# Optimization experiments

Hardware: AMD Instinct MI355X
Metric: run time of the kernel (lower is better)

## Reference

```python
import jax, jax.numpy as jnp
import numpy as np
import math

V, S, D, B = 50257, 2048, 512, 4
DFF = 4 * D
EPS = 1e-5


def layer_norm(z, g, b):
    mu = jnp.mean(z, axis=-1, keepdims=True)
    var = jnp.mean((z - mu) ** 2, axis=-1, keepdims=True)
    return (z - mu) * jax.lax.rsqrt(var + EPS) * g + b


def pos_embedding(seq_len, d_model):
    # Faithful to get_positional_value: angle = pos / 10000**(2*i/d), sin for even i, cos for odd i
    pos = jnp.arange(seq_len, dtype=jnp.float32)[:, None]          # [S,1]
    i = jnp.arange(d_model, dtype=jnp.float32)[None, :]            # [1,D]
    ang = pos / jnp.power(10000.0, 2.0 * i / d_model)              # [S,D]
    even = (jnp.arange(d_model) % 2 == 0)[None, :]
    return jnp.where(even, jnp.sin(ang), jnp.cos(ang))


def setup_inputs() -> dict:
    key = jax.random.key(0)
    ks = jax.random.split(key, 14)
    w = lambda k, sh: jax.random.normal(k, sh, dtype=jnp.float32) * 0.02
    return {
        "input_seq": jax.random.randint(ks[0], (B, S), 0, V),
        "emb": w(ks[1], (V, D)),
        "wk": w(ks[2], (D, D)), "bk": jnp.zeros((D,), jnp.float32),
        "wq": w(ks[3], (D, D)), "bq": jnp.zeros((D,), jnp.float32),
        "wv": w(ks[4], (D, D)), "bv": jnp.zeros((D,), jnp.float32),
        "ln_g": jnp.ones((D,), jnp.float32), "ln_b": jnp.zeros((D,), jnp.float32),
        "w1": w(ks[5], (D, DFF)), "b1": jnp.zeros((DFF,), jnp.float32),
        "w2": w(ks[6], (DFF, D)), "b2": jnp.zeros((D,), jnp.float32),
    }


def reference(input_seq, emb, wk, bk, wq, bq, wv, bv, ln_g, ln_b, w1, b1, w2, b2):
    x = emb[input_seq]                                              # [B,S,D]
    x = (x + pos_embedding(S, D)) * math.sqrt(D)
    # NB original passes (k, q, v) into Attention(Q, K, V), so Q:=k_proj, K:=q_proj, V:=v_proj
    k = x @ wk + bk
    q = x @ wq + bq
    v = x @ wv + bv
    scores = jnp.einsum("bid,bjd->bij", k, q) / math.sqrt(D)        # [B,S,S]
    attn = jax.nn.softmax(scores, axis=-1) @ v                      # [B,S,D]
    r = layer_norm(x + attn, ln_g, ln_b)
    ff = jax.nn.gelu(r @ w1 + b1, approximate=False) @ w2 + b2
    out = layer_norm(r + ff, ln_g, ln_b)                            # shared LN params (same module reused)
    return out
```

## Files before the change

kernel.cpp:

```cpp
#include <hip/hip_runtime.h>
#include <math.h>

static constexpr int BB  = 4;
static constexpr int S   = 2048;
static constexpr int D   = 512;
static constexpr int DFF = 2048;
static constexpr int BS  = BB * S;

using v8h = __attribute__((ext_vector_type(8))) _Float16;
using v4h = __attribute__((ext_vector_type(4))) _Float16;
using v2h = __attribute__((ext_vector_type(2))) _Float16;
using v4f = __attribute__((ext_vector_type(4))) float;

__device__ __forceinline__ void async16(const void* g, void* l) {
  __builtin_amdgcn_global_load_lds(
      (const __attribute__((address_space(1))) unsigned int*)g,
      (__attribute__((address_space(3))) unsigned int*)l, 16, 0, 0);
}

__device__ __forceinline__ float blockSum(float v) {
#pragma unroll
  for (int o = 32; o; o >>= 1) v += __shfl_xor(v, o, 64);
  __shared__ float t[4];
  __syncthreads();
  if ((threadIdx.x & 63) == 0) t[threadIdx.x >> 6] = v;
  __syncthreads();
  return t[0] + t[1] + t[2] + t[3];
}
__device__ __forceinline__ float blockMax(float v) {
#pragma unroll
  for (int o = 32; o; o >>= 1) v = fmaxf(v, __shfl_xor(v, o, 64));
  __shared__ float t[4];
  __syncthreads();
  if ((threadIdx.x & 63) == 0) t[threadIdx.x >> 6] = v;
  __syncthreads();
  return fmaxf(fmaxf(t[0], t[1]), fmaxf(t[2], t[3]));
}

__global__ __launch_bounds__(256) void embed_pos_k(
    const int* __restrict__ seq, const float* __restrict__ emb,
    float* __restrict__ X, _Float16* __restrict__ Xh) {
  const int bs = blockIdx.x;
  const int s  = bs & (S - 1);
  const int idx = seq[bs];
  const float* er = emb + (size_t)idx * D;
  const float cexp = -0.05190512648261504f;
  const int d0 = threadIdx.x * 2;
  const float2 e2 = *(const float2*)&er[d0];
  const float a0 = (float)s * exp2f((float)d0 * cexp);
  const float a1 = (float)s * exp2f((float)(d0 + 1) * cexp);
  const float v0 = (e2.x + sinf(a0)) * 22.62741699796952f;
  const float v1 = (e2.y + cosf(a1)) * 22.62741699796952f;
  const size_t o = (size_t)bs * D + d0;
  *(float2*)&X[o] = make_float2(v0, v1);
  *(v2h*)&Xh[o] = v2h{(_Float16)v0, (_Float16)v1};
}

__global__ __launch_bounds__(256) void prep_k(
    const float* __restrict__ wk, const float* __restrict__ wq,
    const float* __restrict__ wv, const float* __restrict__ w1,
    const float* __restrict__ w2, const float* __restrict__ bk,
    const float* __restrict__ bq, const float* __restrict__ bv,
    _Float16* __restrict__ wcat, _Float16* __restrict__ w1T,
    _Float16* __restrict__ w2T, float* __restrict__ bcat) {
  const int idx = blockIdx.x * 256 + threadIdx.x;
  if (idx < 786432) {
    const int which = idx >> 18, e = idx & 262143;
    const int k = e >> 9, n = e & 511;
    const float* w = (which == 0) ? wk : (which == 1) ? wq : wv;
    wcat[((long)(which * 512 + n)) * 512 + k] = (_Float16)w[e];
  } else if (idx < 786432 + 1048576) {
    const int e = idx - 786432;
    const int k = e >> 11, n = e & 2047;
    w1T[(long)n * 512 + k] = (_Float16)w1[e];
  } else if (idx < 786432 + 2097152) {
    const int e = idx - 786432 - 1048576;
    const int k = e >> 9, n = e & 511;
    w2T[(long)n * 2048 + k] = (_Float16)w2[e];
  } else if (idx < 786432 + 2097152 + 1536) {
    const int e = idx - 786432 - 2097152;
    const float* b = (e < 512) ? bk : (e < 1024) ? bq : bv;
    bcat[e] = b[e & 511];
  }
}

template <int TM, int OMODE, int ACT>
__global__ __launch_bounds__(256) void mm_k(
    const _Float16* __restrict__ Ap, const _Float16* __restrict__ Bp,
    void* __restrict__ Cp, void* __restrict__ Cp2, void* __restrict__ Cp3,
    const float* __restrict__ bias,
    int N, int K, long sA, long sB, long sC, float scale) {
  constexpr int ATE = TM * 64;
  constexpr int BTE = 128 * 64;
  constexpr int TILE = ATE + BTE;
  __shared__ __align__(16) _Float16 lds[2 * TILE];

  const int tid = threadIdx.x, lane = tid & 63, w = tid >> 6;
  const int quad = lane >> 4, l16 = lane & 15;
  constexpr int MT = 4;
  constexpr int NT = (TM == 128) ? 4 : 2;
  constexpr int WN = (TM == 128) ? 64 : 32;
  const int wm = (TM == 128) ? (w >> 1) : 0;
  const int wn = (TM == 128) ? (w & 1) : w;
  const int m0 = blockIdx.y * TM, n0 = blockIdx.x * 128;

  const _Float16* A = Ap + (long)blockIdx.z * sA;
  const _Float16* B = Bp + (long)blockIdx.z * sB;

  v4f acc[MT][NT] = {};
  const int srow8 = lane >> 3;
  const int cs = (lane & 7) ^ srow8;
  const int lsw = l16 & 7;

  auto stage = [&](int k0, int half) {
    _Float16* Ah = lds + half * TILE;
    _Float16* Bh = Ah + ATE;
#pragma unroll
    for (int i = 0; i < TM / 32; ++i) {
      const int is = w + i * 4;
      async16(A + (long)(m0 + is * 8 + srow8) * K + k0 + cs * 8, Ah + is * 512);
    }
#pragma unroll
    for (int i = 0; i < 4; ++i) {
      const int is = w + i * 4;
      async16(B + (long)(n0 + is * 8 + srow8) * K + k0 + cs * 8, Bh + is * 512);
    }
  };

  stage(0, 0);
  __syncthreads();

  const int nK = K >> 6;
  for (int t = 0; t < nK; ++t) {
    const int cur = t & 1;
    if (t + 1 < nK) stage((t + 1) << 6, cur ^ 1);

    const _Float16* Ah = lds + cur * TILE;
    const _Float16* Bh = Ah + ATE;

    v8h af[MT][2], bfr[NT][2];
#pragma unroll
    for (int mt = 0; mt < MT; ++mt) {
      const int rr = wm * 64 + mt * 16 + l16;
#pragma unroll
      for (int kk = 0; kk < 2; ++kk) {
        const int c = (kk * 4 + quad) ^ lsw;
        af[mt][kk] = *(v8h*)&Ah[rr * 64 + c * 8];
      }
    }
#pragma unroll
    for (int nt = 0; nt < NT; ++nt) {
      const int rn = wn * WN + nt * 16 + l16;
#pragma unroll
      for (int kk = 0; kk < 2; ++kk) {
        const int c = (kk * 4 + quad) ^ lsw;
        bfr[nt][kk] = *(v8h*)&Bh[rn * 64 + c * 8];
      }
    }
#pragma unroll
    for (int kk = 0; kk < 2; ++kk)
#pragma unroll
      for (int mt = 0; mt < MT; ++mt)
#pragma unroll
        for (int nt = 0; nt < NT; ++nt)
          acc[mt][nt] = __builtin_amdgcn_mfma_f32_16x16x32_f16(
              af[mt][kk], bfr[nt][kk], acc[mt][nt], 0, 0, 0);

    __syncthreads();
  }

  const long Cz = (long)blockIdx.z * sC;
  const int region = n0 >> 9;
#pragma unroll
  for (int nt = 0; nt < NT; ++nt) {
    const int gn = n0 + wn * WN + nt * 16 + l16;
    const int gnl = gn & 511;
    const float bv = bias ? bias[gn] : 0.0f;
#pragma unroll
    for (int mt = 0; mt < MT; ++mt) {
      const int gmb = m0 + wm * 64 + mt * 16 + quad * 4;
      if constexpr (OMODE == 4) {
        if (region == 2) {
          const int z2 = gmb >> 11, ml = gmb & 2047;
          v4h h4;
#pragma unroll
          for (int r = 0; r < 4; ++r)
            h4[r] = (_Float16)(acc[mt][nt][r] * scale + bv);
          *(v4h*)&((_Float16*)Cp3)[((long)z2 * 512 + gnl) * 2048 + ml] = h4;
          continue;
        }
      }
#pragma unroll
      for (int r = 0; r < 4; ++r) {
        const int gm = gmb + r;
        float v = acc[mt][nt][r] * scale + bv;
        if constexpr (ACT == 1)
          v = 0.5f * v * (1.0f + erff(v * 0.7071067811865476f));
        if constexpr (OMODE == 0) {
          ((float*)Cp)[Cz + (long)gm * N + gn] = v;
        } else if constexpr (OMODE == 1) {
          ((_Float16*)Cp)[Cz + (long)gm * N + gn] = (_Float16)v;
        } else {
          if (region == 0) {
            ((_Float16*)Cp)[(long)gm * 512 + gnl] = (_Float16)v;
          } else {
            ((_Float16*)Cp2)[(long)gm * 512 + gnl] = (_Float16)v;
          }
        }
      }
    }
  }
}

__global__ __launch_bounds__(256) void mm64p_k(
    const _Float16* __restrict__ Ap, const _Float16* __restrict__ Bp,
    float* __restrict__ Cp, const float* __restrict__ bias,
    int N, int K, long sA, long sB, long sC, float scale) {
  constexpr int ATE = 64 * 64;
  constexpr int BTE = 128 * 64;
  constexpr int TILE = ATE + BTE;
  __shared__ __align__(16) _Float16 lds[3 * TILE];

  const int tid = threadIdx.x, lane = tid & 63, w = tid >> 6;
  const int quad = lane >> 4, l16 = lane & 15;
  const int m0 = blockIdx.y * 64, n0 = blockIdx.x * 128;

  const _Float16* A = Ap + (long)blockIdx.z * sA;
  const _Float16* B = Bp + (long)blockIdx.z * sB;

  v4f acc[4][2] = {};
  const int srow8 = lane >> 3;
  const int cs = (lane & 7) ^ srow8;
  const int lsw = l16 & 7;

  auto stage = [&](int t) {
    _Float16* Ah = lds + (t % 3) * TILE;
    _Float16* Bh = Ah + ATE;
    const int k0 = t << 6;
#pragma unroll
    for (int i = 0; i < 2; ++i) {
      const int is = w + i * 4;
      async16(A + (long)(m0 + is * 8 + srow8) * K + k0 + cs * 8, Ah + is * 512);
    }
#pragma unroll
    for (int i = 0; i < 4; ++i) {
      const int is = w + i * 4;
      async16(B + (long)(n0 + is * 8 + srow8) * K + k0 + cs * 8, Bh + is * 512);
    }
  };

  const int nK = K >> 6;
  stage(0);
  stage(1);

  for (int t = 0; t < nK; ++t) {
    __builtin_amdgcn_s_barrier();
    if (t + 2 < nK) {
      stage(t + 2);
      asm volatile("s_waitcnt vmcnt(12)" ::: "memory");
    } else if (t + 1 < nK) {
      asm volatile("s_waitcnt vmcnt(6)" ::: "memory");
    } else {
      asm volatile("s_waitcnt vmcnt(0)" ::: "memory");
    }
    __builtin_amdgcn_s_barrier();

    const _Float16* Ah = lds + (t % 3) * TILE;
    const _Float16* Bh = Ah + ATE;

    v8h af[4][2], bfr[2][2];
#pragma unroll
    for (int mt = 0; mt < 4; ++mt) {
      const int rr = mt * 16 + l16;
#pragma unroll
      for (int kk = 0; kk < 2; ++kk) {
        const int c = (kk * 4 + quad) ^ lsw;
        af[mt][kk] = *(v8h*)&Ah[rr * 64 + c * 8];
      }
    }
#pragma unroll
    for (int nt = 0; nt < 2; ++nt) {
      const int rn = w * 32 + nt * 16 + l16;
#pragma unroll
      for (int kk = 0; kk < 2; ++kk) {
        const int c = (kk * 4 + quad) ^ lsw;
        bfr[nt][kk] = *(v8h*)&Bh[rn * 64 + c * 8];
      }
    }
#pragma unroll
    for (int kk = 0; kk < 2; ++kk)
#pragma unroll
      for (int mt = 0; mt < 4; ++mt)
#pragma unroll
        for (int nt = 0; nt < 2; ++nt)
          acc[mt][nt] = __builtin_amdgcn_mfma_f32_16x16x32_f16(
              af[mt][kk], bfr[nt][kk], acc[mt][nt], 0, 0, 0);
  }

  const long Cz = (long)blockIdx.z * sC;
#pragma unroll
  for (int nt = 0; nt < 2; ++nt) {
    const int gn = n0 + w * 32 + nt * 16 + l16;
    const float bv = bias ? bias[gn] : 0.0f;
#pragma unroll
    for (int mt = 0; mt < 4; ++mt) {
      const int gmb = m0 + mt * 16 + quad * 4;
#pragma unroll
      for (int r = 0; r < 4; ++r) {
        const int gm = gmb + r;
        Cp[Cz + (long)gm * N + gn] = acc[mt][nt][r] * scale + bv;
      }
    }
  }
}

__global__ __launch_bounds__(256) void softmax_k(_Float16* __restrict__ Sc) {
  _Float16* p = Sc + (size_t)blockIdx.x * S;
  const int base = threadIdx.x * 8;
  const v8h a = *(const v8h*)(p + base);
  float v[8];
#pragma unroll
  for (int i = 0; i < 8; ++i) v[i] = (float)a[i];
  float m = -1e30f;
#pragma unroll
  for (int i = 0; i < 8; ++i) m = fmaxf(m, v[i]);
  m = blockMax(m);
  float sum = 0.f;
#pragma unroll
  for (int i = 0; i < 8; ++i) {
    v[i] = exp2f((v[i] - m) * 1.44269504f);
    sum += v[i];
  }
  sum = blockSum(sum);
  const float inv = 1.0f / sum;
  v8h o;
#pragma unroll
  for (int i = 0; i < 8; ++i) o[i] = (_Float16)(v[i] * inv);
  *(v8h*)(p + base) = o;
}

__global__ __launch_bounds__(256) void ln_res_k(
    float* __restrict__ X, const float* __restrict__ Add,
    const float* __restrict__ g, const float* __restrict__ b,
    _Float16* __restrict__ rF) {
  float* xr = X + (size_t)blockIdx.x * D;
  const float* ar = Add + (size_t)blockIdx.x * D;
  _Float16* rf = rF + (size_t)blockIdx.x * D;
  const int d0 = threadIdx.x * 2;
  const float2 xv = *(const float2*)&xr[d0];
  const float2 av = *(const float2*)&ar[d0];
  const float z0 = xv.x + av.x;
  const float z1 = xv.y + av.y;
  const float mu = blockSum(z0 + z1) * (1.0f / D);
  const float dd0 = z0 - mu, dd1 = z1 - mu;
  const float var = blockSum(dd0 * dd0 + dd1 * dd1) * (1.0f / D);
  const float rs = rsqrtf(var + 1e-5f);
  const float2 gv = *(const float2*)&g[d0];
  const float2 bv = *(const float2*)&b[d0];
  const float v0 = dd0 * rs * gv.x + bv.x;
  const float v1 = dd1 * rs * gv.y + bv.y;
  *(float2*)&xr[d0] = make_float2(v0, v1);
  *(v2h*)&rf[d0] = v2h{(_Float16)v0, (_Float16)v1};
}

__global__ __launch_bounds__(256) void ln_out_k(
    const float* __restrict__ R, const float* __restrict__ F,
    const float* __restrict__ g, const float* __restrict__ b,
    float* __restrict__ out) {
  const float* rr = R + (size_t)blockIdx.x * D;
  const float* fr = F + (size_t)blockIdx.x * D;
  float* orow = out + (size_t)blockIdx.x * D;
  const int d0 = threadIdx.x * 2;
  const float2 rv = *(const float2*)&rr[d0];
  const float2 fv = *(const float2*)&fr[d0];
  const float z0 = rv.x + fv.x;
  const float z1 = rv.y + fv.y;
  const float mu = blockSum(z0 + z1) * (1.0f / D);
  const float dd0 = z0 - mu, dd1 = z1 - mu;
  const float var = blockSum(dd0 * dd0 + dd1 * dd1) * (1.0f / D);
  const float rs = rsqrtf(var + 1e-5f);
  const float2 gv = *(const float2*)&g[d0];
  const float2 bv = *(const float2*)&b[d0];
  *(float2*)&orow[d0] =
      make_float2(dd0 * rs * gv.x + bv.x, dd1 * rs * gv.y + bv.y);
}

extern "C" void kernel_launch(void* const* d_in, const int* in_sizes, int n_in,
                              void* d_out, int out_size, void* d_ws, size_t ws_size,
                              hipStream_t stream) {
  (void)in_sizes; (void)n_in; (void)out_size; (void)ws_size;
  const int*   seq = (const int*)d_in[0];
  const float* emb = (const float*)d_in[1];
  const float* wk  = (const float*)d_in[2];
  const float* bk  = (const float*)d_in[3];
  const float* wq  = (const float*)d_in[4];
  const float* bq  = (const float*)d_in[5];
  const float* wv  = (const float*)d_in[6];
  const float* bv  = (const float*)d_in[7];
  const float* lng = (const float*)d_in[8];
  const float* lnb = (const float*)d_in[9];
  const float* w1  = (const float*)d_in[10];
  const float* b1  = (const float*)d_in[11];
  const float* w2  = (const float*)d_in[12];
  const float* b2  = (const float*)d_in[13];

  const size_t MBy = 1024 * 1024;
  char* wsb = (char*)d_ws;
  float*    X    = (float*)wsb;
  _Float16* Xh   = (_Float16*)(wsb + 16 * MBy);
  _Float16* kF   = (_Float16*)(wsb + 24 * MBy);
  _Float16* qF   = (_Float16*)(wsb + 32 * MBy);
  _Float16* vT   = (_Float16*)(wsb + 40 * MBy);
  _Float16* Sc   = (_Float16*)(wsb + 48 * MBy);
  float*    attn = (float*)(wsb + 81 * MBy);
  _Float16* rF   = (_Float16*)(wsb + 24 * MBy);
  _Float16* hF   = (_Float16*)(wsb + 48 * MBy);
  float*    ff   = (float*)(wsb + 32 * MBy);
  _Float16* wcat = (_Float16*)(wsb + 100 * MBy);
  float*    bcat = (float*)(wsb + 102 * MBy);
  _Float16* w1T  = (_Float16*)(wsb + 103 * MBy);
  _Float16* w2T  = (_Float16*)(wsb + 105 * MBy);

  const long SD = (long)S * D, SSl = (long)S * S;

  prep_k<<<11270, 256, 0, stream>>>(wk, wq, wv, w1, w2, bk, bq, bv,
                                    wcat, w1T, w2T, bcat);
  embed_pos_k<<<BS, 256, 0, stream>>>(seq, emb, X, Xh);

  mm_k<128, 4, 0><<<dim3(12, 64, 1), 256, 0, stream>>>(
      Xh, wcat, kF, qF, vT, bcat, 1536, D, 0, 0, 0, 1.0f);

  mm_k<128, 1, 0><<<dim3(16, 16, BB), 256, 0, stream>>>(
      kF, qF, Sc, nullptr, nullptr, nullptr, S, D, SD, SD, SSl,
      0.044194173824159216f);

  softmax_k<<<BS, 256, 0, stream>>>(Sc);

  mm64p_k<<<dim3(4, 32, BB), 256, 0, stream>>>(
      Sc, vT, attn, nullptr, D, S, SSl, (long)D * S, SD, 1.0f);

  ln_res_k<<<BS, 256, 0, stream>>>(X, attn, lng, lnb, rF);

  mm_k<128, 1, 1><<<dim3(16, 64, 1), 256, 0, stream>>>(
      rF, w1T, hF, nullptr, nullptr, b1, DFF, D, 0, 0, 0, 1.0f);
  mm64p_k<<<dim3(4, 128, 1), 256, 0, stream>>>(
      hF, w2T, ff, b2, D, DFF, 0, 0, 0, 1.0f);

  ln_out_k<<<BS, 256, 0, stream>>>(X, ff, lng, lnb, (float*)d_out);
}
```

Measured before the change: 365.6 us.

## Replace 128-tile GEMM with 256x256 tile, 512-thread kernel and vmcnt-based pipelining

After: 427.6 us. 16.9% more time.

```diff
diff --git a/kernel.cpp b/kernel.cpp
--- a/kernel.cpp
+++ b/kernel.cpp
@@ -84,73 +84,62 @@
   }
 }
 
-template <int TM, int OMODE, int ACT>
-__global__ __launch_bounds__(256) void mm_k(
+template <int OMODE, int ACT>
+__global__ __launch_bounds__(512, 2) void mm256p_k(
     const _Float16* __restrict__ Ap, const _Float16* __restrict__ Bp,
     void* __restrict__ Cp, void* __restrict__ Cp2, void* __restrict__ Cp3,
     const float* __restrict__ bias,
     int N, int K, long sA, long sB, long sC, float scale) {
-  constexpr int ATE = TM * 64;
-  constexpr int BTE = 128 * 64;
-  constexpr int TILE = ATE + BTE;
+  constexpr int ATE = 256 * 64;
+  constexpr int TILE = 2 * ATE;
   __shared__ __align__(16) _Float16 lds[2 * TILE];
 
   const int tid = threadIdx.x, lane = tid & 63, w = tid >> 6;
   const int quad = lane >> 4, l16 = lane & 15;
-  constexpr int MT = 4;
-  constexpr int NT = (TM == 128) ? 4 : 2;
-  constexpr int WN = (TM == 128) ? 64 : 32;
-  const int wm = (TM == 128) ? (w >> 1) : 0;
-  const int wn = (TM == 128) ? (w & 1) : w;
-  const int m0 = blockIdx.y * TM, n0 = blockIdx.x * 128;
+  const int wm = w >> 2, wn = w & 3;
+  const int m0 = blockIdx.y * 256, n0 = blockIdx.x * 256;
 
   const _Float16* A = Ap + (long)blockIdx.z * sA;
   const _Float16* B = Bp + (long)blockIdx.z * sB;
 
-  v4f acc[MT][NT] = {};
+  v4f acc[8][4] = {};
   const int srow8 = lane >> 3;
   const int cs = (lane & 7) ^ srow8;
   const int lsw = l16 & 7;
 
-  auto stage = [&](int k0, int half) {
+  auto stage = [&](int t, int half) {
     _Float16* Ah = lds + half * TILE;
     _Float16* Bh = Ah + ATE;
-#pragma unroll
-    for (int i = 0; i < TM / 32; ++i) {
-      const int is = w + i * 4;
+    const int k0 = t << 6;
+#pragma unroll
+    for (int i = 0; i < 4; ++i) {
+      const int is = w + i * 8;
       async16(A + (long)(m0 + is * 8 + srow8) * K + k0 + cs * 8, Ah + is * 512);
-    }
-#pragma unroll
-    for (int i = 0; i < 4; ++i) {
-      const int is = w + i * 4;
       async16(B + (long)(n0 + is * 8 + srow8) * K + k0 + cs * 8, Bh + is * 512);
     }
   };
 
   stage(0, 0);
-  __syncthreads();
 
   const int nK = K >> 6;
   for (int t = 0; t < nK; ++t) {
     const int cur = t & 1;
-    if (t + 1 < nK) stage((t + 1) << 6, cur ^ 1);
+    __builtin_amdgcn_s_barrier();
+    if (t + 1 < nK) {
+      stage(t + 1, cur ^ 1);
+      asm volatile("s_waitcnt vmcnt(8)" ::: "memory");
+    } else {
+      asm volatile("s_waitcnt vmcnt(0)" ::: "memory");
+    }
+    __builtin_amdgcn_s_barrier();
 
     const _Float16* Ah = lds + cur * TILE;
     const _Float16* Bh = Ah + ATE;
 
-    v8h af[MT][2], bfr[NT][2];
-#pragma unroll
-    for (int mt = 0; mt < MT; ++mt) {
-      const int rr = wm * 64 + mt * 16 + l16;
-#pragma unroll
-      for (int kk = 0; kk < 2; ++kk) {
-        const int c = (kk * 4 + quad) ^ lsw;
-        af[mt][kk] = *(v8h*)&Ah[rr * 64 + c * 8];
-      }
-    }
-#pragma unroll
-    for (int nt = 0; nt < NT; ++nt) {
-      const int rn = wn * WN + nt * 16 + l16;
+    v8h bfr[4][2];
+#pragma unroll
+    for (int nt = 0; nt < 4; ++nt) {
+      const int rn = wn * 64 + nt * 16 + l16;
 #pragma unroll
       for (int kk = 0; kk < 2; ++kk) {
         const int c = (kk * 4 + quad) ^ lsw;
@@ -158,27 +147,33 @@
       }
     }
 #pragma unroll
-    for (int kk = 0; kk < 2; ++kk)
-#pragma unroll
-      for (int mt = 0; mt < MT; ++mt)
-#pragma unroll
-        for (int nt = 0; nt < NT; ++nt)
+    for (int mt = 0; mt < 8; ++mt) {
+      const int rr = wm * 128 + mt * 16 + l16;
+      v8h af[2];
+#pragma unroll
+      for (int kk = 0; kk < 2; ++kk) {
+        const int c = (kk * 4 + quad) ^ lsw;
+        af[kk] = *(v8h*)&Ah[rr * 64 + c * 8];
+      }
+#pragma unroll
+      for (int kk = 0; kk < 2; ++kk)
+#pragma unroll
+        for (int nt = 0; nt < 4; ++nt)
           acc[mt][nt] = __builtin_amdgcn_mfma_f32_16x16x32_f16(
-              af[mt][kk], bfr[nt][kk], acc[mt][nt], 0, 0, 0);
-
-    __syncthreads();
+              af[kk], bfr[nt][kk], acc[mt][nt], 0, 0, 0);
+    }
   }
 
   const long Cz = (long)blockIdx.z * sC;
   const int region = n0 >> 9;
 #pragma unroll
-  for (int nt = 0; nt < NT; ++nt) {
-    const int gn = n0 + wn * WN + nt * 16 + l16;
+  for (int nt = 0; nt < 4; ++nt) {
+    const int gn = n0 + wn * 64 + nt * 16 + l16;
     const int gnl = gn & 511;
     const float bv = bias ? bias[gn] : 0.0f;
 #pragma unroll
-    for (int mt = 0; mt < MT; ++mt) {
-      const int gmb = m0 + wm * 64 + mt * 16 + quad * 4;
+    for (int mt = 0; mt < 8; ++mt) {
+      const int gmb = m0 + wm * 128 + mt * 16 + quad * 4;
       if constexpr (OMODE == 4) {
         if (region == 2) {
           const int z2 = gmb >> 11, ml = gmb & 2047;
@@ -196,9 +191,7 @@
         float v = acc[mt][nt][r] * scale + bv;
         if constexpr (ACT == 1)
           v = 0.5f * v * (1.0f + erff(v * 0.7071067811865476f));
-        if constexpr (OMODE == 0) {
-          ((float*)Cp)[Cz + (long)gm * N + gn] = v;
-        } else if constexpr (OMODE == 1) {
+        if constexpr (OMODE == 1) {
           ((_Float16*)Cp)[Cz + (long)gm * N + gn] = (_Float16)v;
         } else {
           if (region == 0) {
@@ -427,10 +420,10 @@
                                     wcat, w1T, w2T, bcat);
   embed_pos_k<<<BS, 256, 0, stream>>>(seq, emb, X, Xh);
 
-  mm_k<128, 4, 0><<<dim3(12, 64, 1), 256, 0, stream>>>(
+  mm256p_k<4, 0><<<dim3(6, 32, 1), 512, 0, stream>>>(
       Xh, wcat, kF, qF, vT, bcat, 1536, D, 0, 0, 0, 1.0f);
 
-  mm_k<128, 1, 0><<<dim3(16, 16, BB), 256, 0, stream>>>(
+  mm256p_k<1, 0><<<dim3(8, 8, BB), 512, 0, stream>>>(
       kF, qF, Sc, nullptr, nullptr, nullptr, S, D, SD, SD, SSl,
       0.044194173824159216f);
 
@@ -441,7 +434,7 @@
 
   ln_res_k<<<BS, 256, 0, stream>>>(X, attn, lng, lnb, rF);
 
-  mm_k<128, 1, 1><<<dim3(16, 64, 1), 256, 0, stream>>>(
+  mm256p_k<1, 1><<<dim3(8, 32, 1), 512, 0, stream>>>(
       rF, w1T, hF, nullptr, nullptr, b1, DFF, D, 0, 0, 0, 1.0f);
   mm64p_k<<<dim3(4, 128, 1), 256, 0, stream>>>(
       hF, w2T, ff, b2, D, DFF, 0, 0, 0, 1.0f);
```
